# Kernel optimization log

Hardware: AMD Instinct MI355X
Metric: run time of the kernel (lower is better)

The kernel has to match this reference:

```python
import jax, jax.numpy as jnp
import numpy as np

MARGIN = 0.3
NUM_CLASSES = 32  # includes label 0, which the mask logic treats specially


def setup_inputs() -> dict:
    key = jax.random.key(0)
    k1, k2 = jax.random.split(key)
    n, d = 4096, 2048
    inputs = jax.random.normal(k1, (n, d), dtype=jnp.float32)
    targets = jax.random.randint(k2, (n,), 0, NUM_CLASSES, dtype=jnp.int64)
    return {"inputs": inputs, "targets": targets}


def reference(inputs, targets):
    # Pairwise euclidean distance matrix [n, n]
    sq = jnp.sum(inputs * inputs, axis=1)  # [n]
    dist2 = sq[:, None] + sq[None, :] - 2.0 * (inputs @ inputs.T)
    dist = jnp.sqrt(jnp.maximum(dist2, 1e-12))

    # Mask semantics from the torch code:
    #   mask == 1  : same label (hard-positive pool; includes diagonal)
    #   mask == 0  : different labels AND at least one of the pair has label 0
    #   mask == -1 : different labels, both nonzero (excluded from mining)
    ti, tj = targets[:, None], targets[None, :]
    same = ti == tj
    zero_neg = (~same) & ((ti == 0) | (tj == 0))

    neg_inf = jnp.asarray(-jnp.inf, dist.dtype)
    pos_inf = jnp.asarray(jnp.inf, dist.dtype)
    dist_ap = jnp.max(jnp.where(same, dist, neg_inf), axis=1)      # hardest positive per row
    row_min = jnp.min(jnp.where(zero_neg, dist, pos_inf), axis=1)  # hardest label-0 negative

    # Torch code checks row 0 only (mask[0]) for the presence of mask==0 entries;
    # if row 0 has none, ALL dist_an are set to 0. Reproduce faithfully.
    row0_has_zero = jnp.any(zero_neg[0])
    dist_an = jnp.where(row0_has_zero, row_min, jnp.zeros_like(row_min))

    # MarginRankingLoss with y = 1: mean(relu(-(dist_an - dist_ap) + margin))
    loss = jnp.mean(jax.nn.relu(dist_ap - dist_an + MARGIN))
    return loss
```

## Files before the change

### kernel.cpp

```cpp
#include <hip/hip_runtime.h>
#include <hip/hip_bf16.h>
#include <math.h>

#define N 4096
#define K 2048
#define NC 32
#define MARGIN 0.3f

#define BK 128
#define NITER (K / BK)
#define DIAG_BLOCKS 192
#define CROSS_BLOCKS 192
#define GRID (DIAG_BLOCKS + CROSS_BLOCKS)

typedef float f32x4 __attribute__((ext_vector_type(4)));
typedef __bf16 bf16x8 __attribute__((ext_vector_type(8)));

__device__ __forceinline__ void glds16(const void* g, void* l) {
  __builtin_amdgcn_global_load_lds(
      (const __attribute__((address_space(1))) void*)g,
      (__attribute__((address_space(3))) void*)l, 16, 0, 0);
}

__device__ __forceinline__ int imin(int a, int b) { return a < b ? a : b; }

__global__ __launch_bounds__(256) void convert_kernel(
    const float* __restrict__ X, const int* __restrict__ tg,
    __bf16* __restrict__ Xg, float* __restrict__ sqg,
    unsigned int* __restrict__ ap, unsigned int* __restrict__ an,
    int* __restrict__ cnt, int* __restrict__ off, int* __restrict__ flag,
    int* __restrict__ done) {
  __shared__ int h[NC];
  int t = threadIdx.x;
  int w = t >> 6, lane = t & 63;
  int row = blockIdx.x * 4 + w;
  const float4* xr = (const float4*)(X + (size_t)row * K);

  float4 v[8];
  #pragma unroll
  for (int q = 0; q < 4; q++) {
    int chunk = q * 64 + lane;
    v[2 * q]     = xr[chunk * 2];
    v[2 * q + 1] = xr[chunk * 2 + 1];
  }

  int c = tg[row];
  const int4* tg4 = (const int4*)tg;
  int pc = 0;
  #pragma unroll 4
  for (int chunk = lane; chunk < N / 4; chunk += 64) {
    int4 tv = tg4[chunk];
    int base = chunk * 4;
    pc += (tv.x < c) + ((tv.x == c) & (base + 0 < row));
    pc += (tv.y < c) + ((tv.y == c) & (base + 1 < row));
    pc += (tv.z < c) + ((tv.z == c) & (base + 2 < row));
    pc += (tv.w < c) + ((tv.w == c) & (base + 3 < row));
  }

  float s = 0.f;
  bf16x8 b[4];
  #pragma unroll
  for (int q = 0; q < 4; q++) {
    float4 a0 = v[2 * q], a1 = v[2 * q + 1];
    s += a0.x * a0.x + a0.y * a0.y + a0.z * a0.z + a0.w * a0.w +
         a1.x * a1.x + a1.y * a1.y + a1.z * a1.z + a1.w * a1.w;
    b[q][0] = (__bf16)a0.x; b[q][1] = (__bf16)a0.y;
    b[q][2] = (__bf16)a0.z; b[q][3] = (__bf16)a0.w;
    b[q][4] = (__bf16)a1.x; b[q][5] = (__bf16)a1.y;
    b[q][6] = (__bf16)a1.z; b[q][7] = (__bf16)a1.w;
  }

  #pragma unroll
  for (int m = 32; m; m >>= 1) {
    s += __shfl_xor(s, m);
    pc += __shfl_xor(pc, m);
  }
  int pos = pc;

  bf16x8* dst = (bf16x8*)(Xg + (size_t)pos * K);
  #pragma unroll
  for (int q = 0; q < 4; q++) dst[q * 64 + lane] = b[q];

  if (lane == 0) {
    sqg[pos] = s;
    ap[pos] = 0u;
    an[pos] = 0x7f800000u;
  }

  if (blockIdx.x == 0) {
    if (t < NC) h[t] = 0;
    __syncthreads();
    for (int i = t; i < N / 4; i += 256) {
      int4 v4 = tg4[i];
      atomicAdd(&h[v4.x], 1); atomicAdd(&h[v4.y], 1);
      atomicAdd(&h[v4.z], 1); atomicAdd(&h[v4.w], 1);
    }
    __syncthreads();
    if (t == 0) {
      int acc = 0;
      for (int cc = 0; cc < NC; cc++) {
        cnt[cc] = h[cc];
        off[cc] = acc;
        acc += h[cc];
      }
      int t0 = tg[0];
      flag[0] = (t0 == 0) ? (N - h[0] > 0) : (h[0] > 0);
      done[0] = 0;
    }
  }
}

__global__ __launch_bounds__(256) void gemm_reduce_kernel(
    const __bf16* __restrict__ Xg, const float* __restrict__ sqg,
    const int* __restrict__ cnt, const int* __restrict__ off,
    unsigned int* __restrict__ ap, unsigned int* __restrict__ an,
    const int* __restrict__ flag, int* __restrict__ done,
    float* __restrict__ out) {
  __shared__ __align__(16) __bf16 sA[2][64 * BK];
  __shared__ __align__(16) __bf16 sB[2][64 * BK];
  __shared__ int s_islast;
  __shared__ float wred[4];

  int b = blockIdx.x;
  int t = threadIdx.x;

  bool active = true, diag = true, dcol = false;
  int i0g = 0, iend = 1, j0g = 0, jend = 1;
  if (b < DIAG_BLOCKS) {
    int c = b / 6, p = b % 6;
    int sti = (p < 3) ? 0 : (p < 5 ? 1 : 2);
    int stj = (p < 3) ? p : (p < 5 ? p - 2 : 2);
    int o = off[c], n = cnt[c];
    if (n == 0 || sti * 64 >= n || stj * 64 >= n) active = false;
    i0g = o + sti * 64; iend = o + n;
    j0g = o + stj * 64; jend = o + n;
    dcol = (sti != stj);
  } else {
    int idx = b - DIAG_BLOCKS;
    int it = idx >> 6, jt = idx & 63;
    int n0 = cnt[0];
    int j0 = n0 + jt * 64;
    if (n0 == 0 || it * 64 >= n0 || j0 >= N) active = false;
    i0g = it * 64; iend = n0;
    j0g = j0; jend = N;
    diag = false;
  }

  if (active) {
    int w = t >> 6, l = t & 63;
    int wi = w >> 1, wj = w & 1;
    int quad = l >> 4, lr = l & 15;

    const char* gA[4]; const char* gB[4];
    int rr = t >> 4, cbl = t & 15;
    int cbg = cbl ^ rr;
    #pragma unroll
    for (int r = 0; r < 4; r++) {
      int row_l = r * 16 + rr;
      int ra = imin(i0g + row_l, iend - 1);
      int rb = imin(j0g + row_l, jend - 1);
      gA[r] = (const char*)(Xg + (size_t)ra * K) + cbg * 16;
      gB[r] = (const char*)(Xg + (size_t)rb * K) + cbg * 16;
    }

    int aoff[2][4], boff[2][4];
    #pragma unroll
    for (int ti = 0; ti < 2; ti++)
      #pragma unroll
      for (int kc = 0; kc < 4; kc++) {
        int cb = kc * 4 + quad;
        int sw = (cb ^ lr) * 16;
        aoff[ti][kc] = (wi * 32 + ti * 16 + lr) * 256 + sw;
        boff[ti][kc] = (wj * 32 + ti * 16 + lr) * 256 + sw;
      }

    f32x4 acc[2][2];
    acc[0][0] = (f32x4)0.f; acc[0][1] = (f32x4)0.f;
    acc[1][0] = (f32x4)0.f; acc[1][1] = (f32x4)0.f;

    auto stage = [&](int buf, int itk) {
      int koff = itk * (BK * 2);
      char* la = (char*)sA + buf * 16384 + t * 16;
      char* lb = (char*)sB + buf * 16384 + t * 16;
      #pragma unroll
      for (int r = 0; r < 4; r++) {
        glds16(gA[r] + koff, la + r * 4096);
        glds16(gB[r] + koff, lb + r * 4096);
      }
    };

    auto compute = [&](int buf) {
      const char* bufA = (const char*)sA + buf * 16384;
      const char* bufB = (const char*)sB + buf * 16384;
      #pragma unroll
      for (int kc = 0; kc < 4; kc++) {
        bf16x8 a0 = *(const bf16x8*)(bufA + aoff[0][kc]);
        bf16x8 a1 = *(const bf16x8*)(bufA + aoff[1][kc]);
        bf16x8 b0 = *(const bf16x8*)(bufB + boff[0][kc]);
        bf16x8 b1 = *(const bf16x8*)(bufB + boff[1][kc]);
        acc[0][0] = __builtin_amdgcn_mfma_f32_16x16x32_bf16(a0, b0, acc[0][0], 0, 0, 0);
        acc[0][1] = __builtin_amdgcn_mfma_f32_16x16x32_bf16(a0, b1, acc[0][1], 0, 0, 0);
        acc[1][0] = __builtin_amdgcn_mfma_f32_16x16x32_bf16(a1, b0, acc[1][0], 0, 0, 0);
        acc[1][1] = __builtin_amdgcn_mfma_f32_16x16x32_bf16(a1, b1, acc[1][1], 0, 0, 0);
      }
    };

    stage(0, 0);
    for (int itk = 0; itk < NITER - 1; ++itk) {
      int cur = itk & 1;
      __builtin_amdgcn_s_barrier();
      stage(cur ^ 1, itk + 1);
      __builtin_amdgcn_s_waitcnt(0x0F78);
      __builtin_amdgcn_s_barrier();
      __builtin_amdgcn_sched_barrier(0);
      compute(cur);
    }
    __builtin_amdgcn_s_barrier();
    __builtin_amdgcn_s_waitcnt(0x0F70);
    __builtin_amdgcn_s_barrier();
    __builtin_amdgcn_sched_barrier(0);
    compute((NITER - 1) & 1);

    int jgc[2]; float sqj[2];
    #pragma unroll
    for (int tj = 0; tj < 2; tj++) {
      int jg = j0g + wj * 32 + tj * 16 + lr;
      jgc[tj] = imin(jg, jend - 1);
      sqj[tj] = sqg[jgc[tj]];
    }

    if (diag) {
      float colmax[2] = {0.f, 0.f};
      #pragma unroll
      for (int ti = 0; ti < 2; ti++) {
        #pragma unroll
        for (int r = 0; r < 4; r++) {
          int ig = i0g + wi * 32 + ti * 16 + quad * 4 + r;
          int igc = imin(ig, iend - 1);
          float sqi = sqg[igc];
          float apm = 0.f;
          #pragma unroll
          for (int tj = 0; tj < 2; tj++) {
            float d2 = sqi + sqj[tj] - 2.f * acc[ti][tj][r];
            float d = sqrtf(fmaxf(d2, 1e-12f));
            apm = fmaxf(apm, d);
            colmax[tj] = fmaxf(colmax[tj], d);
          }
          #pragma unroll
          for (int m = 1; m < 16; m <<= 1) apm = fmaxf(apm, __shfl_xor(apm, m));
          if (lr == 0) atomicMax(ap + igc, __float_as_uint(apm));
        }
      }
      if (dcol) {
        #pragma unroll
        for (int tj = 0; tj < 2; tj++) {
          float v = colmax[tj];
          v = fmaxf(v, __shfl_xor(v, 16));
          v = fmaxf(v, __shfl_xor(v, 32));
          if (quad == 0) atomicMax(ap + jgc[tj], __float_as_uint(v));
        }
      }
    } else {
      float colmin[2] = {INFINITY, INFINITY};
      #pragma unroll
      for (int ti = 0; ti < 2; ti++) {
        #pragma unroll
        for (int r = 0; r < 4; r++) {
          int ig = i0g + wi * 32 + ti * 16 + quad * 4 + r;
          int igc = imin(ig, iend - 1);
          float sqi = sqg[igc];
          float anm = INFINITY;
          #pragma unroll
          for (int tj = 0; tj < 2; tj++) {
            float d2 = sqi + sqj[tj] - 2.f * acc[ti][tj][r];
            float d = sqrtf(fmaxf(d2, 1e-12f));
            anm = fminf(anm, d);
            colmin[tj] = fminf(colmin[tj], d);
          }
          #pragma unroll
          for (int m = 1; m < 16; m <<= 1) anm = fminf(anm, __shfl_xor(anm, m));
          if (lr == 0) atomicMin(an + igc, __float_as_uint(anm));
        }
      }
      #pragma unroll
      for (int tj = 0; tj < 2; tj++) {
        float v = colmin[tj];
        v = fminf(v, __shfl_xor(v, 16));
        v = fminf(v, __shfl_xor(v, 32));
        if (quad == 0) atomicMin(an + jgc[tj], __float_as_uint(v));
      }
    }
  }

  __syncthreads();
  if (t == 0) {
    __threadfence();
    int ticket = __hip_atomic_fetch_add(done, 1, __ATOMIC_ACQ_REL,
                                        __HIP_MEMORY_SCOPE_AGENT);
    s_islast = (ticket == GRID - 1);
  }
  __syncthreads();
  if (s_islast) {
    int has = flag[0];
    float s = 0.f;
    for (int i = t; i < N; i += 256) {
      unsigned int au = __hip_atomic_load(ap + i, __ATOMIC_RELAXED,
                                          __HIP_MEMORY_SCOPE_AGENT);
      unsigned int nu = __hip_atomic_load(an + i, __ATOMIC_RELAXED,
                                          __HIP_MEMORY_SCOPE_AGENT);
      float a = __uint_as_float(au);
      float bb = has ? __uint_as_float(nu) : 0.f;
      s += fmaxf(a - bb + MARGIN, 0.f);
    }
    #pragma unroll
    for (int m = 32; m; m >>= 1) s += __shfl_xor(s, m);
    if ((t & 63) == 0) wred[t >> 6] = s;
    __syncthreads();
    if (t == 0) out[0] = (wred[0] + wred[1] + wred[2] + wred[3]) / (float)N;
  }
}

extern "C" void kernel_launch(void* const* d_in, const int* in_sizes, int n_in,
                              void* d_out, int out_size, void* d_ws,
                              size_t ws_size, hipStream_t stream) {
  const float* X = (const float*)d_in[0];
  const int* tg = (const int*)d_in[1];
  float* out = (float*)d_out;

  char* ws = (char*)d_ws;
  __bf16* Xg = (__bf16*)ws;
  size_t o = (size_t)N * K * 2;
  float* sqg = (float*)(ws + o); o += (size_t)N * 4;
  unsigned int* ap = (unsigned int*)(ws + o); o += (size_t)N * 4;
  unsigned int* an = (unsigned int*)(ws + o); o += (size_t)N * 4;
  int* cnt = (int*)(ws + o); o += NC * 4;
  int* off = (int*)(ws + o); o += NC * 4;
  int* flag = (int*)(ws + o); o += 4;
  int* done = (int*)(ws + o); o += 4;

  convert_kernel<<<N / 4, 256, 0, stream>>>(X, tg, Xg, sqg, ap, an, cnt, off,
                                            flag, done);
  gemm_reduce_kernel<<<GRID, 256, 0, stream>>>(Xg, sqg, cnt, off, ap, an,
                                               flag, done, out);
}
```

Measured before the change: 117.9 us.

## Fuse convert and GEMM-reduce into one persistent kernel with a grid barrier

```diff
diff --git a/kernel.cpp b/kernel.cpp
--- a/kernel.cpp
+++ b/kernel.cpp
@@ -24,67 +24,74 @@
 
 __device__ __forceinline__ int imin(int a, int b) { return a < b ? a : b; }
 
-__global__ __launch_bounds__(256) void convert_kernel(
+__global__ __launch_bounds__(256, 2) void fused_kernel(
     const float* __restrict__ X, const int* __restrict__ tg,
     __bf16* __restrict__ Xg, float* __restrict__ sqg,
     unsigned int* __restrict__ ap, unsigned int* __restrict__ an,
     int* __restrict__ cnt, int* __restrict__ off, int* __restrict__ flag,
-    int* __restrict__ done) {
+    int* __restrict__ ctrl, float* __restrict__ out) {
+  __shared__ __align__(16) __bf16 sA[2][64 * BK];
+  __shared__ __align__(16) __bf16 sB[2][64 * BK];
   __shared__ int h[NC];
+  __shared__ int s_islast;
+  __shared__ float wred[4];
+
   int t = threadIdx.x;
   int w = t >> 6, lane = t & 63;
-  int row = blockIdx.x * 4 + w;
-  const float4* xr = (const float4*)(X + (size_t)row * K);
-
-  float4 v[8];
-  #pragma unroll
-  for (int q = 0; q < 4; q++) {
-    int chunk = q * 64 + lane;
-    v[2 * q]     = xr[chunk * 2];
-    v[2 * q + 1] = xr[chunk * 2 + 1];
-  }
-
-  int c = tg[row];
   const int4* tg4 = (const int4*)tg;
-  int pc = 0;
-  #pragma unroll 4
-  for (int chunk = lane; chunk < N / 4; chunk += 64) {
-    int4 tv = tg4[chunk];
-    int base = chunk * 4;
-    pc += (tv.x < c) + ((tv.x == c) & (base + 0 < row));
-    pc += (tv.y < c) + ((tv.y == c) & (base + 1 < row));
-    pc += (tv.z < c) + ((tv.z == c) & (base + 2 < row));
-    pc += (tv.w < c) + ((tv.w == c) & (base + 3 < row));
-  }
-
-  float s = 0.f;
-  bf16x8 b[4];
-  #pragma unroll
-  for (int q = 0; q < 4; q++) {
-    float4 a0 = v[2 * q], a1 = v[2 * q + 1];
-    s += a0.x * a0.x + a0.y * a0.y + a0.z * a0.z + a0.w * a0.w +
-         a1.x * a1.x + a1.y * a1.y + a1.z * a1.z + a1.w * a1.w;
-    b[q][0] = (__bf16)a0.x; b[q][1] = (__bf16)a0.y;
-    b[q][2] = (__bf16)a0.z; b[q][3] = (__bf16)a0.w;
-    b[q][4] = (__bf16)a1.x; b[q][5] = (__bf16)a1.y;
-    b[q][6] = (__bf16)a1.z; b[q][7] = (__bf16)a1.w;
-  }
-
-  #pragma unroll
-  for (int m = 32; m; m >>= 1) {
-    s += __shfl_xor(s, m);
-    pc += __shfl_xor(pc, m);
-  }
-  int pos = pc;
-
-  bf16x8* dst = (bf16x8*)(Xg + (size_t)pos * K);
-  #pragma unroll
-  for (int q = 0; q < 4; q++) dst[q * 64 + lane] = b[q];
-
-  if (lane == 0) {
-    sqg[pos] = s;
-    ap[pos] = 0u;
-    an[pos] = 0x7f800000u;
+
+  for (int row = blockIdx.x * 4 + w; row < N; row += GRID * 4) {
+    const float4* xr = (const float4*)(X + (size_t)row * K);
+
+    float4 v[8];
+    #pragma unroll
+    for (int q = 0; q < 4; q++) {
+      int chunk = q * 64 + lane;
+      v[2 * q]     = xr[chunk * 2];
+      v[2 * q + 1] = xr[chunk * 2 + 1];
+    }
+
+    int c = tg[row];
+    int pc = 0;
+    #pragma unroll 4
+    for (int chunk = lane; chunk < N / 4; chunk += 64) {
+      int4 tv = tg4[chunk];
+      int base = chunk * 4;
+      pc += (tv.x < c) + ((tv.x == c) & (base + 0 < row));
+      pc += (tv.y < c) + ((tv.y == c) & (base + 1 < row));
+      pc += (tv.z < c) + ((tv.z == c) & (base + 2 < row));
+      pc += (tv.w < c) + ((tv.w == c) & (base + 3 < row));
+    }
+
+    float s = 0.f;
+    bf16x8 b[4];
+    #pragma unroll
+    for (int q = 0; q < 4; q++) {
+      float4 a0 = v[2 * q], a1 = v[2 * q + 1];
+      s += a0.x * a0.x + a0.y * a0.y + a0.z * a0.z + a0.w * a0.w +
+           a1.x * a1.x + a1.y * a1.y + a1.z * a1.z + a1.w * a1.w;
+      b[q][0] = (__bf16)a0.x; b[q][1] = (__bf16)a0.y;
+      b[q][2] = (__bf16)a0.z; b[q][3] = (__bf16)a0.w;
+      b[q][4] = (__bf16)a1.x; b[q][5] = (__bf16)a1.y;
+      b[q][6] = (__bf16)a1.z; b[q][7] = (__bf16)a1.w;
+    }
+
+    #pragma unroll
+    for (int m = 32; m; m >>= 1) {
+      s += __shfl_xor(s, m);
+      pc += __shfl_xor(pc, m);
+    }
+    int pos = pc;
+
+    bf16x8* dst = (bf16x8*)(Xg + (size_t)pos * K);
+    #pragma unroll
+    for (int q = 0; q < 4; q++) dst[q * 64 + lane] = b[q];
+
+    if (lane == 0) {
+      sqg[pos] = s;
+      ap[pos] = 0u;
+      an[pos] = 0x7f800000u;
+    }
   }
 
   if (blockIdx.x == 0) {
@@ -105,24 +112,21 @@
       }
       int t0 = tg[0];
       flag[0] = (t0 == 0) ? (N - h[0] > 0) : (h[0] > 0);
-      done[0] = 0;
-    }
-  }
-}
-
-__global__ __launch_bounds__(256) void gemm_reduce_kernel(
-    const __bf16* __restrict__ Xg, const float* __restrict__ sqg,
-    const int* __restrict__ cnt, const int* __restrict__ off,
-    unsigned int* __restrict__ ap, unsigned int* __restrict__ an,
-    const int* __restrict__ flag, int* __restrict__ done,
-    float* __restrict__ out) {
-  __shared__ __align__(16) __bf16 sA[2][64 * BK];
-  __shared__ __align__(16) __bf16 sB[2][64 * BK];
-  __shared__ int s_islast;
-  __shared__ float wred[4];
+    }
+  }
+
+  __syncthreads();
+  if (t == 0) {
+    __threadfence();
+    __hip_atomic_fetch_add(&ctrl[0], 1, __ATOMIC_ACQ_REL,
+                           __HIP_MEMORY_SCOPE_AGENT);
+    while (__hip_atomic_load(&ctrl[0], __ATOMIC_ACQUIRE,
+                             __HIP_MEMORY_SCOPE_AGENT) < GRID)
+      __builtin_amdgcn_s_sleep(2);
+  }
+  __syncthreads();
 
   int b = blockIdx.x;
-  int t = threadIdx.x;
 
   bool active = true, diag = true, dcol = false;
   int i0g = 0, iend = 1, j0g = 0, jend = 1;
@@ -147,7 +151,7 @@
   }
 
   if (active) {
-    int w = t >> 6, l = t & 63;
+    int l = t & 63;
     int wi = w >> 1, wj = w & 1;
     int quad = l >> 4, lr = l & 15;
 
@@ -295,7 +299,7 @@
   __syncthreads();
   if (t == 0) {
     __threadfence();
-    int ticket = __hip_atomic_fetch_add(done, 1, __ATOMIC_ACQ_REL,
+    int ticket = __hip_atomic_fetch_add(&ctrl[1], 1, __ATOMIC_ACQ_REL,
                                         __HIP_MEMORY_SCOPE_AGENT);
     s_islast = (ticket == GRID - 1);
   }
@@ -336,10 +340,9 @@
   int* cnt = (int*)(ws + o); o += NC * 4;
   int* off = (int*)(ws + o); o += NC * 4;
   int* flag = (int*)(ws + o); o += 4;
-  int* done = (int*)(ws + o); o += 4;
-
-  convert_kernel<<<N / 4, 256, 0, stream>>>(X, tg, Xg, sqg, ap, an, cnt, off,
-                                            flag, done);
-  gemm_reduce_kernel<<<GRID, 256, 0, stream>>>(Xg, sqg, cnt, off, ap, an,
-                                               flag, done, out);
+  int* ctrl = (int*)(ws + o); o += 8;
+
+  hipMemsetAsync(ctrl, 0, 8, stream);
+  fused_kernel<<<GRID, 256, 0, stream>>>(X, tg, Xg, sqg, ap, an, cnt, off,
+                                         flag, ctrl, out);
 }
```

Measured after the change: 184.3 us. +56.3%, slower.
